# Optimization experiments

Hardware: AMD Instinct MI355X
Metric: run time of the kernel (lower is better)

Reference implementation:

```python
import jax, jax.numpy as jnp
import numpy as np

CAPACITY_FACTOR = 1.2


def setup_inputs() -> dict:
    key = jax.random.key(0)
    k1, k2, k3 = jax.random.split(key, 3)
    B, S, D, E = 8, 4096, 512, 16
    x = jax.random.normal(k1, (B, S, D), dtype=jnp.float32)
    switch_w = jax.random.normal(k2, (E, D), dtype=jnp.float32) * 0.02
    switch_b = jnp.zeros((E,), dtype=jnp.float32)
    expert_w = jax.random.normal(k3, (E, D, D), dtype=jnp.float32) * 0.02
    expert_b = jnp.zeros((E, D), dtype=jnp.float32)
    return {"x": x, "switch_w": switch_w, "switch_b": switch_b,
            "expert_w": expert_w, "expert_b": expert_b}


def reference(x, switch_w, switch_b, expert_w, expert_b):
    B, S, D = x.shape
    E = switch_w.shape[0]
    N = B * S
    xf = x.reshape(N, D)

    # Router: softmax over experts, top-1 route.
    logits = xf @ switch_w.T + switch_b            # [N, E]
    probs = jax.nn.softmax(logits, axis=-1)
    route_probs = jnp.max(probs, axis=-1)          # [N]
    routes = jnp.argmax(probs, axis=-1)            # [N] int

    # Position of each token within its expert's queue (token order).
    oh = jax.nn.one_hot(routes, E, dtype=jnp.int32)            # [N, E]
    pos = jnp.take_along_axis(jnp.cumsum(oh, axis=0), routes[:, None], axis=1)[:, 0] - 1  # [N]

    capacity = int(CAPACITY_FACTOR * N / E)        # static
    keep = pos < capacity                          # [N] bool; overflow tokens dropped

    # Dispatch: scatter kept tokens into [E, capacity, D] buffer.
    # Out-of-capacity positions are out-of-bounds and dropped by scatter semantics.
    buf = jnp.zeros((E, capacity, D), dtype=xf.dtype).at[routes, pos].set(xf)

    # Per-expert Linear (torch Linear: y = x @ W.T + b), as one grouped GEMM.
    y = jnp.einsum('ecd,efd->ecf', buf, expert_w) + expert_b[:, None, :]  # [E, C, D]

    # Combine: gather expert outputs back; dropped tokens pass through x.
    gathered = y[routes, jnp.minimum(pos, capacity - 1)]       # [N, D]
    out = jnp.where(keep[:, None], gathered, xf) * route_probs[:, None]
    return out.reshape(B, S, D)
```

## Files before the change

### kernel.cpp

```cpp
#include <hip/hip_runtime.h>
#include <math.h>

#define N_TOK 32768
#define DIM   512
#define NEXP  16
#define CAP   2457
#define CAPP  2464
#define NCHUNK 512

typedef __attribute__((ext_vector_type(8))) short   short8;
typedef __attribute__((ext_vector_type(4))) short   short4v;
typedef __attribute__((ext_vector_type(4))) float   floatx4;

__device__ __forceinline__ short f2bf(float f) {
  unsigned u = __builtin_bit_cast(unsigned, f);
  unsigned r = u + 0x7FFFu + ((u >> 16) & 1u);
  return (short)(r >> 16);
}
__device__ __forceinline__ float bf2f(short h) {
  return __builtin_bit_cast(float, ((unsigned)(unsigned short)h) << 16);
}

#define LGP 17
__global__ __launch_bounds__(256) void router_k(
    const float* __restrict__ x, const float* __restrict__ sw,
    const float* __restrict__ sb, const float* __restrict__ ew,
    int* __restrict__ route, float* __restrict__ prob, int* __restrict__ hist,
    short* __restrict__ x_bf, short* __restrict__ w_bf) {
  __shared__ short swh[16][520];
  __shared__ short swl[16][520];
  __shared__ float lgt[64][LGP];
  __shared__ float sbs[NEXP];

  int tid = threadIdx.x;

  {
    const float4* src = (const float4*)ew;
    short4v* dst = (short4v*)w_bf;
    int base = blockIdx.x * 2048 + tid;
#pragma unroll
    for (int i = 0; i < 8; ++i) {
      float4 f = src[base + i * 256];
      short4v s;
      s[0] = f2bf(f.x); s[1] = f2bf(f.y); s[2] = f2bf(f.z); s[3] = f2bf(f.w);
      dst[base + i * 256] = s;
    }
  }

  {
    int idx = tid;
#pragma unroll
    for (int i = 0; i < 8; ++i, idx += 256) {
      int e = idx >> 7, k4 = idx & 127;
      float4 f = ((const float4*)(sw + e * DIM))[k4];
      short4v h, l;
      h[0] = f2bf(f.x); h[1] = f2bf(f.y); h[2] = f2bf(f.z); h[3] = f2bf(f.w);
      l[0] = f2bf(f.x - bf2f(h[0]));
      l[1] = f2bf(f.y - bf2f(h[1]));
      l[2] = f2bf(f.z - bf2f(h[2]));
      l[3] = f2bf(f.w - bf2f(h[3]));
      *(short4v*)&swh[e][k4 * 4] = h;
      *(short4v*)&swl[e][k4 * 4] = l;
    }
  }
  if (tid < NEXP) sbs[tid] = sb[tid];
  __syncthreads();

  int wv = tid >> 6, lane = tid & 63, q = lane >> 4, l16 = lane & 15;
  int row = blockIdx.x * 64 + wv * 16 + l16;
  const float* xr = x + (size_t)row * DIM;
  short* xbr = x_bf + (size_t)row * DIM;

  floatx4 acc = {};
#pragma unroll 4
  for (int kc = 0; kc < 16; ++kc) {
    int k0 = kc * 32 + q * 8;
    float4 f0 = *(const float4*)(xr + k0);
    float4 f1 = *(const float4*)(xr + k0 + 4);
    short8 hi, lo;
    hi[0] = f2bf(f0.x); hi[1] = f2bf(f0.y); hi[2] = f2bf(f0.z); hi[3] = f2bf(f0.w);
    hi[4] = f2bf(f1.x); hi[5] = f2bf(f1.y); hi[6] = f2bf(f1.z); hi[7] = f2bf(f1.w);
    lo[0] = f2bf(f0.x - bf2f(hi[0])); lo[1] = f2bf(f0.y - bf2f(hi[1]));
    lo[2] = f2bf(f0.z - bf2f(hi[2])); lo[3] = f2bf(f0.w - bf2f(hi[3]));
    lo[4] = f2bf(f1.x - bf2f(hi[4])); lo[5] = f2bf(f1.y - bf2f(hi[5]));
    lo[6] = f2bf(f1.z - bf2f(hi[6])); lo[7] = f2bf(f1.w - bf2f(hi[7]));
    *(short8*)(xbr + k0) = hi;
    short8 bh = *(const short8*)&swh[l16][k0];
    short8 bl = *(const short8*)&swl[l16][k0];
    acc = __builtin_amdgcn_mfma_f32_16x16x32_bf16(hi, bh, acc, 0, 0, 0);
    acc = __builtin_amdgcn_mfma_f32_16x16x32_bf16(lo, bh, acc, 0, 0, 0);
    acc = __builtin_amdgcn_mfma_f32_16x16x32_bf16(hi, bl, acc, 0, 0, 0);
  }
#pragma unroll
  for (int r = 0; r < 4; ++r)
    lgt[wv * 16 + q * 4 + r][l16] = acc[r];
  __syncthreads();

  if (tid < 64) {
    int t = blockIdx.x * 64 + tid;
    float lg[NEXP];
#pragma unroll
    for (int e = 0; e < NEXP; ++e) lg[e] = lgt[tid][e] + sbs[e];
    int arg = 0; float mx = lg[0];
#pragma unroll
    for (int e = 1; e < NEXP; ++e)
      if (lg[e] > mx) { mx = lg[e]; arg = e; }
    float s = 0.f;
#pragma unroll
    for (int e = 0; e < NEXP; ++e) s += expf(lg[e] - mx);
    route[t] = arg;
    prob[t]  = 1.0f / s;
#pragma unroll
    for (int e = 0; e < NEXP; ++e) {
      unsigned long long m = __ballot(arg == e);
      if (tid == e) hist[blockIdx.x * NEXP + e] = __popcll(m);
    }
  }
}

__global__ __launch_bounds__(256) void pos_k(
    const int* __restrict__ route, const float* __restrict__ prob,
    const int* __restrict__ hist, const float* __restrict__ x,
    float* __restrict__ out, int* __restrict__ lists,
    int* __restrict__ counts) {
  __shared__ int part[16][NEXP];
  __shared__ int base_s[NEXP];
  __shared__ int wcnt[4][NEXP];
  int tid = threadIdx.x;
  int b = blockIdx.x;
  int c0 = b * 4;
  {
    int g = tid >> 4, e = tid & 15;
    int s = 0;
    for (int c = g; c < c0; c += 16) s += hist[c * NEXP + e];
    part[g][e] = s;
  }
  __syncthreads();
  if (tid < NEXP) {
    int s = 0;
#pragma unroll
    for (int gg = 0; gg < 16; ++gg) s += part[gg][tid];
    base_s[tid] = s;
  }
  int wv = tid >> 6, lane = tid & 63;
  int t = b * 256 + wv * 64 + lane;
  int r = route[t];
  unsigned long long lower = (1ull << lane) - 1ull;
  int rank = 0;
#pragma unroll
  for (int e = 0; e < NEXP; ++e) {
    unsigned long long m = __ballot(r == e);
    if (r == e) rank = __popcll(m & lower);
    if (lane == e) wcnt[wv][e] = __popcll(m);
  }
  __syncthreads();
  int pre = base_s[r];
  for (int w2 = 0; w2 < wv; ++w2) pre += wcnt[w2][r];
  int pos = pre + rank;
  if (pos < CAP) {
    lists[r * CAPP + pos] = t;
  } else {
    float p = prob[t];
    const float4* xr = (const float4*)(x + (size_t)t * DIM);
    float4* o = (float4*)(out + (size_t)t * DIM);
    for (int d = 0; d < DIM / 4; ++d) {
      float4 v = xr[d];
      v.x *= p; v.y *= p; v.z *= p; v.w *= p;
      o[d] = v;
    }
  }
  if (b == 127 && tid < NEXP)
    counts[tid] = base_s[tid] + wcnt[0][tid] + wcnt[1][tid]
                + wcnt[2][tid] + wcnt[3][tid];
}

#define BM 64
#define BN 128
#define BKS 64

__global__ __launch_bounds__(256, 4) void gemm_k(
    const short* __restrict__ x_bf, const short* __restrict__ w_bf,
    const float* __restrict__ eb, const int* __restrict__ lists,
    const int* __restrict__ counts, const float* __restrict__ prob,
    float* __restrict__ out) {
  int e = blockIdx.z;
  int cnt = counts[e]; if (cnt > CAP) cnt = CAP;
  int row0 = blockIdx.y * BM;
  if (row0 >= cnt) return;
  int col0 = blockIdx.x * BN;

  __shared__ short A_s[BM * BKS];
  __shared__ short B_s[BN * BKS];
  __shared__ int rowtok[BM];

  int tid = threadIdx.x;
  if (tid < BM) {
    int gr = row0 + tid;
    rowtok[tid] = (gr < cnt) ? lists[e * CAPP + gr] : 0;
  }
  __syncthreads();

  int wv = tid >> 6, lane = tid & 63;
  int q = lane >> 4, l16 = lane & 15;
  int wrow = (wv >> 1) * 32, wcol = (wv & 1) * 64;

  int r_loc = lane >> 3, c = lane & 7;
  const short* ga[2]; short* la[2];
  const short* gb[4]; short* lb[4];
#pragma unroll
  for (int t2 = 0; t2 < 2; ++t2) {
    int row = wv * 16 + t2 * 8 + r_loc;
    int g = c ^ (row & 7);
    ga[t2] = x_bf + (size_t)rowtok[row] * DIM + g * 8;
    la[t2] = &A_s[(wv * 16 + t2 * 8) * BKS];
  }
#pragma unroll
  for (int t4 = 0; t4 < 4; ++t4) {
    int row = wv * 32 + t4 * 8 + r_loc;
    int g = c ^ (row & 7);
    gb[t4] = w_bf + (size_t)(e * DIM + col0 + row) * DIM + g * 8;
    lb[t4] = &B_s[(wv * 32 + t4 * 8) * BKS];
  }

  floatx4 acc[2][4] = {};

  for (int k0 = 0; k0 < DIM; k0 += BKS) {
#pragma unroll
    for (int t2 = 0; t2 < 2; ++t2)
      __builtin_amdgcn_global_load_lds(
          (const __attribute__((address_space(1))) void*)(ga[t2] + k0),
          (__attribute__((address_space(3))) void*)(la[t2]), 16, 0, 0);
#pragma unroll
    for (int t4 = 0; t4 < 4; ++t4)
      __builtin_amdgcn_global_load_lds(
          (const __attribute__((address_space(1))) void*)(gb[t4] + k0),
          (__attribute__((address_space(3))) void*)(lb[t4]), 16, 0, 0);
    __syncthreads();
#pragma unroll
    for (int kk = 0; kk < 2; ++kk) {
      short8 af[2], bfv[4];
      int ckbase = kk * 4 + q;
#pragma unroll
      for (int sm = 0; sm < 2; ++sm) {
        int row = wrow + sm * 16 + l16;
        int ph = ckbase ^ (row & 7);
        af[sm] = *(const short8*)&A_s[row * BKS + ph * 8];
      }
#pragma unroll
      for (int sn = 0; sn < 4; ++sn) {
        int row = wcol + sn * 16 + l16;
        int ph = ckbase ^ (row & 7);
        bfv[sn] = *(const short8*)&B_s[row * BKS + ph * 8];
      }
#pragma unroll
      for (int sm = 0; sm < 2; ++sm)
#pragma unroll
        for (int sn = 0; sn < 4; ++sn)
          acc[sm][sn] = __builtin_amdgcn_mfma_f32_16x16x32_bf16(
              af[sm], bfv[sn], acc[sm][sn], 0, 0, 0);
    }
    __syncthreads();
  }

#pragma unroll
  for (int sm = 0; sm < 2; ++sm) {
    int tt[4]; float pp[4]; int vld[4];
#pragma unroll
    for (int rg = 0; rg < 4; ++rg) {
      int rr = wrow + sm * 16 + q * 4 + rg;
      int gr = row0 + rr;
      vld[rg] = (gr < cnt);
      tt[rg]  = rowtok[rr];
      pp[rg]  = vld[rg] ? prob[tt[rg]] : 0.f;
    }
#pragma unroll
    for (int sn = 0; sn < 4; ++sn) {
      int col = col0 + wcol + sn * 16 + l16;
      float bias = eb[e * DIM + col];
#pragma unroll
      for (int rg = 0; rg < 4; ++rg)
        if (vld[rg])
          out[(size_t)tt[rg] * DIM + col] = (acc[sm][sn][rg] + bias) * pp[rg];
    }
  }
}

extern "C" void kernel_launch(void* const* d_in, const int* in_sizes, int n_in,
                              void* d_out, int out_size, void* d_ws, size_t ws_size,
                              hipStream_t stream) {
  const float* x  = (const float*)d_in[0];
  const float* sw = (const float*)d_in[1];
  const float* sb = (const float*)d_in[2];
  const float* ew = (const float*)d_in[3];
  const float* eb = (const float*)d_in[4];
  float* out = (float*)d_out;

  char* ws = (char*)d_ws;
  int*   route  = (int*)(ws + 0);
  float* prob   = (float*)(ws + 131072);
  int*   hist   = (int*)(ws + 262144);
  int*   counts = (int*)(ws + 327680);
  int*   lists  = (int*)(ws + 327744);
  short* x_bf   = (short*)(ws + (1 << 20));
  short* w_bf   = (short*)(ws + (1 << 20) + 33554432);

  hipLaunchKernelGGL(router_k, dim3(NCHUNK), dim3(256), 0, stream,
                     x, sw, sb, ew, route, prob, hist, x_bf, w_bf);
  hipLaunchKernelGGL(pos_k, dim3(128), dim3(256), 0, stream,
                     route, prob, hist, x, out, lists, counts);
  hipLaunchKernelGGL(gemm_k, dim3(4, 39, 16), dim3(256), 0, stream,
                     x_bf, w_bf, eb, lists, counts, prob, out);
}
```

Baseline: 181.9 us.

## Double-buffer GEMM LDS tiles and remap workgroups across XCDs

The GEMM now keeps two LDS stages, so the global-to-LDS load of the next K tile is issued before the MFMAs on the current tile, overlapping memory latency with compute. The 3D grid becomes a 1D grid of 2496 workgroups. Each id is remapped so consecutive tiles of the same expert land on the same XCD (8 XCDs, 312 each), which should improve L2 reuse of expert weights and token rows. LDS use per block doubles and launch bounds drop to 3 blocks per CU, which reduces occupancy.

Measured after the change: 191.8 us. +5.4%, slower.

```diff
diff --git a/kernel.cpp b/kernel.cpp
--- a/kernel.cpp
+++ b/kernel.cpp
@@ -177,20 +177,71 @@
 #define BM 64
 #define BN 128
 #define BKS 64
-
-__global__ __launch_bounds__(256, 4) void gemm_k(
+#define NWG_G 2496
+#define CPX_G 312
+
+#define GEMM_STAGE(b, k0)                                                     \
+  {                                                                           \
+    _Pragma("unroll")                                                         \
+    for (int t2 = 0; t2 < 2; ++t2)                                            \
+      __builtin_amdgcn_global_load_lds(                                       \
+          (const __attribute__((address_space(1))) void*)(ga[t2] + (k0)),     \
+          (__attribute__((address_space(3))) void*)(la[t2] + (b) * (BM*BKS)), \
+          16, 0, 0);                                                          \
+    _Pragma("unroll")                                                         \
+    for (int t4 = 0; t4 < 4; ++t4)                                            \
+      __builtin_amdgcn_global_load_lds(                                       \
+          (const __attribute__((address_space(1))) void*)(gb[t4] + (k0)),     \
+          (__attribute__((address_space(3))) void*)(lb[t4] + (b) * (BN*BKS)), \
+          16, 0, 0);                                                          \
+  }
+
+#define GEMM_COMPUTE(b)                                                       \
+  {                                                                           \
+    _Pragma("unroll")                                                         \
+    for (int kk = 0; kk < 2; ++kk) {                                          \
+      short8 af[2], bfv[4];                                                   \
+      int ckbase = kk * 4 + q;                                                \
+      _Pragma("unroll")                                                       \
+      for (int sm = 0; sm < 2; ++sm) {                                        \
+        int row = wrow + sm * 16 + l16;                                       \
+        int ph = ckbase ^ (row & 7);                                          \
+        af[sm] = *(const short8*)&A_s[b][row * BKS + ph * 8];                 \
+      }                                                                       \
+      _Pragma("unroll")                                                       \
+      for (int sn = 0; sn < 4; ++sn) {                                        \
+        int row = wcol + sn * 16 + l16;                                       \
+        int ph = ckbase ^ (row & 7);                                          \
+        bfv[sn] = *(const short8*)&B_s[b][row * BKS + ph * 8];                \
+      }                                                                       \
+      _Pragma("unroll")                                                       \
+      for (int sm = 0; sm < 2; ++sm)                                          \
+        _Pragma("unroll")                                                     \
+        for (int sn = 0; sn < 4; ++sn)                                        \
+          acc[sm][sn] = __builtin_amdgcn_mfma_f32_16x16x32_bf16(              \
+              af[sm], bfv[sn], acc[sm][sn], 0, 0, 0);                         \
+    }                                                                         \
+  }
+
+__global__ __launch_bounds__(256, 3) void gemm_k(
     const short* __restrict__ x_bf, const short* __restrict__ w_bf,
     const float* __restrict__ eb, const int* __restrict__ lists,
     const int* __restrict__ counts, const float* __restrict__ prob,
     float* __restrict__ out) {
-  int e = blockIdx.z;
+  int orig = blockIdx.x;
+  int wgid = (orig & 7) * CPX_G + (orig >> 3);
+  int e    = wgid / 156;
+  int rem  = wgid - e * 156;
+  int by   = rem >> 2;
+  int bx   = rem & 3;
+
   int cnt = counts[e]; if (cnt > CAP) cnt = CAP;
-  int row0 = blockIdx.y * BM;
+  int row0 = by * BM;
   if (row0 >= cnt) return;
-  int col0 = blockIdx.x * BN;
-
-  __shared__ short A_s[BM * BKS];
-  __shared__ short B_s[BN * BKS];
+  int col0 = bx * BN;
+
+  __shared__ short A_s[2][BM * BKS];
+  __shared__ short B_s[2][BN * BKS];
   __shared__ int rowtok[BM];
 
   int tid = threadIdx.x;
@@ -212,53 +263,28 @@
     int row = wv * 16 + t2 * 8 + r_loc;
     int g = c ^ (row & 7);
     ga[t2] = x_bf + (size_t)rowtok[row] * DIM + g * 8;
-    la[t2] = &A_s[(wv * 16 + t2 * 8) * BKS];
+    la[t2] = &A_s[0][(wv * 16 + t2 * 8) * BKS];
   }
 #pragma unroll
   for (int t4 = 0; t4 < 4; ++t4) {
     int row = wv * 32 + t4 * 8 + r_loc;
     int g = c ^ (row & 7);
     gb[t4] = w_bf + (size_t)(e * DIM + col0 + row) * DIM + g * 8;
-    lb[t4] = &B_s[(wv * 32 + t4 * 8) * BKS];
+    lb[t4] = &B_s[0][(wv * 32 + t4 * 8) * BKS];
   }
 
   floatx4 acc[2][4] = {};
 
-  for (int k0 = 0; k0 < DIM; k0 += BKS) {
-#pragma unroll
-    for (int t2 = 0; t2 < 2; ++t2)
-      __builtin_amdgcn_global_load_lds(
-          (const __attribute__((address_space(1))) void*)(ga[t2] + k0),
-          (__attribute__((address_space(3))) void*)(la[t2]), 16, 0, 0);
-#pragma unroll
-    for (int t4 = 0; t4 < 4; ++t4)
-      __builtin_amdgcn_global_load_lds(
-          (const __attribute__((address_space(1))) void*)(gb[t4] + k0),
-          (__attribute__((address_space(3))) void*)(lb[t4]), 16, 0, 0);
+  GEMM_STAGE(0, 0);
+  __syncthreads();
+#pragma unroll
+  for (int k0 = 0; k0 < DIM; k0 += 2 * BKS) {
+    GEMM_STAGE(1, k0 + BKS);
+    GEMM_COMPUTE(0);
     __syncthreads();
-#pragma unroll
-    for (int kk = 0; kk < 2; ++kk) {
-      short8 af[2], bfv[4];
-      int ckbase = kk * 4 + q;
-#pragma unroll
-      for (int sm = 0; sm < 2; ++sm) {
-        int row = wrow + sm * 16 + l16;
-        int ph = ckbase ^ (row & 7);
-        af[sm] = *(const short8*)&A_s[row * BKS + ph * 8];
-      }
-#pragma unroll
-      for (int sn = 0; sn < 4; ++sn) {
-        int row = wcol + sn * 16 + l16;
-        int ph = ckbase ^ (row & 7);
-        bfv[sn] = *(const short8*)&B_s[row * BKS + ph * 8];
-      }
-#pragma unroll
-      for (int sm = 0; sm < 2; ++sm)
-#pragma unroll
-        for (int sn = 0; sn < 4; ++sn)
-          acc[sm][sn] = __builtin_amdgcn_mfma_f32_16x16x32_bf16(
-              af[sm], bfv[sn], acc[sm][sn], 0, 0, 0);
-    }
+    if (k0 + 2 * BKS < DIM)
+      GEMM_STAGE(0, k0 + 2 * BKS);
+    GEMM_COMPUTE(1);
     __syncthreads();
   }
 
@@ -308,6 +334,6 @@
                      x, sw, sb, ew, route, prob, hist, x_bf, w_bf);
   hipLaunchKernelGGL(pos_k, dim3(128), dim3(256), 0, stream,
                      route, prob, hist, x, out, lists, counts);
-  hipLaunchKernelGGL(gemm_k, dim3(4, 39, 16), dim3(256), 0, stream,
+  hipLaunchKernelGGL(gemm_k, dim3(NWG_G), dim3(256), 0, stream,
                      x_bf, w_bf, eb, lists, counts, prob, out);
 }
```

## Double GEMM row tile to 128 and remap blocks per XCD

Applied to the files above, without the earlier changes.

The expert GEMM tile grows from 64 to 128 rows, so each wave computes a 4x4 grid of MFMA accumulators and each loaded weight tile is reused across twice as many token rows. The 3D grid becomes a flat 1D grid. Block ids are remapped so that consecutive work for the same expert stays on the same XCD, which should improve L2 reuse of expert weights. The costs are higher register and LDS use (occupancy hint lowered to 3) and more wasted rows in the partially filled last tile of each expert.

Result: no change. 180.7 us (-0.7%).

```diff
diff --git a/kernel.cpp b/kernel.cpp
--- a/kernel.cpp
+++ b/kernel.cpp
@@ -174,20 +174,29 @@
                 + wcnt[2][tid] + wcnt[3][tid];
 }
 
-#define BM 64
+#define BM 128
 #define BN 128
 #define BKS 64
-
-__global__ __launch_bounds__(256, 4) void gemm_k(
+#define TPE 80
+#define NWG_G (TPE * NEXP)
+#define CPX_G (NWG_G / 8)
+
+__global__ __launch_bounds__(256, 3) void gemm_k(
     const short* __restrict__ x_bf, const short* __restrict__ w_bf,
     const float* __restrict__ eb, const int* __restrict__ lists,
     const int* __restrict__ counts, const float* __restrict__ prob,
     float* __restrict__ out) {
-  int e = blockIdx.z;
+  int orig = blockIdx.x;
+  int wgid = (orig & 7) * CPX_G + (orig >> 3);
+  int e    = wgid / TPE;
+  int rem  = wgid - e * TPE;
+  int by   = rem >> 2;
+  int bx   = rem & 3;
+
   int cnt = counts[e]; if (cnt > CAP) cnt = CAP;
-  int row0 = blockIdx.y * BM;
+  int row0 = by * BM;
   if (row0 >= cnt) return;
-  int col0 = blockIdx.x * BN;
+  int col0 = bx * BN;
 
   __shared__ short A_s[BM * BKS];
   __shared__ short B_s[BN * BKS];
@@ -202,34 +211,29 @@
 
   int wv = tid >> 6, lane = tid & 63;
   int q = lane >> 4, l16 = lane & 15;
-  int wrow = (wv >> 1) * 32, wcol = (wv & 1) * 64;
+  int wrow = (wv & 2) * 32, wcol = (wv & 1) * 64;
 
   int r_loc = lane >> 3, c = lane & 7;
-  const short* ga[2]; short* la[2];
+  const short* ga[4]; short* la[4];
   const short* gb[4]; short* lb[4];
-#pragma unroll
-  for (int t2 = 0; t2 < 2; ++t2) {
-    int row = wv * 16 + t2 * 8 + r_loc;
-    int g = c ^ (row & 7);
-    ga[t2] = x_bf + (size_t)rowtok[row] * DIM + g * 8;
-    la[t2] = &A_s[(wv * 16 + t2 * 8) * BKS];
-  }
 #pragma unroll
   for (int t4 = 0; t4 < 4; ++t4) {
     int row = wv * 32 + t4 * 8 + r_loc;
     int g = c ^ (row & 7);
+    ga[t4] = x_bf + (size_t)rowtok[row] * DIM + g * 8;
+    la[t4] = &A_s[(wv * 32 + t4 * 8) * BKS];
     gb[t4] = w_bf + (size_t)(e * DIM + col0 + row) * DIM + g * 8;
     lb[t4] = &B_s[(wv * 32 + t4 * 8) * BKS];
   }
 
-  floatx4 acc[2][4] = {};
+  floatx4 acc[4][4] = {};
 
   for (int k0 = 0; k0 < DIM; k0 += BKS) {
 #pragma unroll
-    for (int t2 = 0; t2 < 2; ++t2)
+    for (int t4 = 0; t4 < 4; ++t4)
       __builtin_amdgcn_global_load_lds(
-          (const __attribute__((address_space(1))) void*)(ga[t2] + k0),
-          (__attribute__((address_space(3))) void*)(la[t2]), 16, 0, 0);
+          (const __attribute__((address_space(1))) void*)(ga[t4] + k0),
+          (__attribute__((address_space(3))) void*)(la[t4]), 16, 0, 0);
 #pragma unroll
     for (int t4 = 0; t4 < 4; ++t4)
       __builtin_amdgcn_global_load_lds(
@@ -238,10 +242,10 @@
     __syncthreads();
 #pragma unroll
     for (int kk = 0; kk < 2; ++kk) {
-      short8 af[2], bfv[4];
+      short8 af[4], bfv[4];
       int ckbase = kk * 4 + q;
 #pragma unroll
-      for (int sm = 0; sm < 2; ++sm) {
+      for (int sm = 0; sm < 4; ++sm) {
         int row = wrow + sm * 16 + l16;
         int ph = ckbase ^ (row & 7);
         af[sm] = *(const short8*)&A_s[row * BKS + ph * 8];
@@ -253,7 +257,7 @@
         bfv[sn] = *(const short8*)&B_s[row * BKS + ph * 8];
       }
 #pragma unroll
-      for (int sm = 0; sm < 2; ++sm)
+      for (int sm = 0; sm < 4; ++sm)
 #pragma unroll
         for (int sn = 0; sn < 4; ++sn)
           acc[sm][sn] = __builtin_amdgcn_mfma_f32_16x16x32_bf16(
@@ -263,7 +267,7 @@
   }
 
 #pragma unroll
-  for (int sm = 0; sm < 2; ++sm) {
+  for (int sm = 0; sm < 4; ++sm) {
     int tt[4]; float pp[4]; int vld[4];
 #pragma unroll
     for (int rg = 0; rg < 4; ++rg) {
@@ -308,6 +312,6 @@
                      x, sw, sb, ew, route, prob, hist, x_bf, w_bf);
   hipLaunchKernelGGL(pos_k, dim3(128), dim3(256), 0, stream,
                      route, prob, hist, x, out, lists, counts);
-  hipLaunchKernelGGL(gemm_k, dim3(4, 39, 16), dim3(256), 0, stream,
+  hipLaunchKernelGGL(gemm_k, dim3(NWG_G), dim3(256), 0, stream,
                      x_bf, w_bf, eb, lists, counts, prob, out);
 }
```
